# Optimization experiments

Hardware: AMD Instinct MI355X
Metric: run time of the kernel (lower is better)

Reference implementation:

```python
import jax, jax.numpy as jnp
import numpy as np

ROBOT_W = 1.0
PHASE_W = 1.0
COHER_W = 10.0
SPEED_W = 5.0
MAX_SPEED = 10.0
SMOOTH_VEL_W = 0.05
SMOOTH_ACC_W = 0.01

# illegal phase transitions {(0,2),(1,0),(2,0),(2,1)} as a 3x3 lookup table
_ILLEGAL = np.zeros((3, 3), dtype=bool)
for a, b in [(0, 2), (1, 0), (2, 0), (2, 1)]:
    _ILLEGAL[a, b] = True
ILLEGAL_TABLE = jnp.asarray(_ILLEGAL)


def setup_inputs() -> dict:
    key = jax.random.key(0)
    k1, k2, k3, k4 = jax.random.split(key, 4)
    B, T = 256, 8192
    # scale by 8 so per-frame speeds (norm of diffs of 3-vectors) exceed MAX_SPEED
    pred_robot = jax.random.normal(k1, (B, T, 12), dtype=jnp.float32) * 8.0
    gt_robot = jax.random.normal(k2, (B, T, 12), dtype=jnp.float32) * 8.0
    pred_phase = jax.random.normal(k3, (B, T, 3), dtype=jnp.float32)
    gt_phase = jax.random.randint(k4, (B, T), 0, 3, dtype=jnp.int32)
    return {"pred_robot": pred_robot, "pred_phase": pred_phase,
            "gt_robot": gt_robot, "gt_phase": gt_phase}


def _coherence_loss(phase_logits):
    # vectorized replacement for the O(B*T) Python double loop
    p = jnp.argmax(phase_logits, axis=-1)            # [B, T]
    pt, pt1 = p[:, :-1], p[:, 1:]                    # [B, T-1]
    illegal = ILLEGAL_TABLE[pt, pt1]                 # [B, T-1] bool
    # logit of the (illegal) predicted phase at t+1
    sel = jnp.take_along_axis(phase_logits[:, 1:], pt1[..., None], axis=-1)[..., 0]
    loss_sum = jnp.sum(jnp.where(illegal, sel * sel, 0.0))
    count = jnp.sum(illegal)
    return jnp.where(count > 0, loss_sum / jnp.maximum(count, 1).astype(sel.dtype), 0.0)


def _speed_loss(pred_robot):
    B, T, D = pred_robot.shape
    vel = pred_robot[:, 1:] - pred_robot[:, :-1]     # [B, T-1, 12]
    pts = vel.reshape(B, T - 1, 4, 3)
    speeds = jnp.linalg.norm(pts, axis=-1)           # [B, T-1, 4]
    pen = jax.nn.relu(speeds - MAX_SPEED)
    return SPEED_W * jnp.mean(pen * pen)


def reference(pred_robot, pred_phase, gt_robot, gt_phase):
    # MSE over robot trajectory
    robot_loss = jnp.mean((pred_robot - gt_robot) ** 2)
    # cross-entropy over 3 phase classes
    logp = jax.nn.log_softmax(pred_phase, axis=-1)   # [B, T, 3]
    nll = -jnp.take_along_axis(logp, gt_phase[..., None].astype(jnp.int32), axis=-1)[..., 0]
    phase_loss = jnp.mean(nll)
    coherence = _coherence_loss(pred_phase)
    speed_loss = _speed_loss(pred_robot)
    vel = pred_robot[:, 1:] - pred_robot[:, :-1]
    vel_loss = jnp.mean(vel * vel)
    acc = pred_robot[:, 2:] - 2.0 * pred_robot[:, 1:-1] + pred_robot[:, :-2]
    acc_loss = jnp.mean(acc * acc)
    total = (ROBOT_W * robot_loss + PHASE_W * phase_loss + COHER_W * coherence
             + speed_loss + SMOOTH_VEL_W * vel_loss + SMOOTH_ACC_W * acc_loss)
    return total
```

## Files before the change

### kernel.cpp

```cpp
#include <hip/hip_runtime.h>
#include <math.h>

#define B_DIM 256
#define T_DIM 8192
#define BLOCK 256
#define NSLOT 256
#define K_PRED 4
#define NPB (BLOCK * K_PRED)
#define NF4 (B_DIM * T_DIM * 3)
#define NPH4 (NF4 / 4)
#define GRID_BLOCKS (NF4 / NPB)


__device__ __forceinline__ unsigned div3u(unsigned x) {
    return __umulhi(x, 0xAAAAAAABu) >> 1;
}
__device__ __forceinline__ float pen_term(float s) {
    float d = fmaxf(sqrtf(s) - 10.0f, 0.0f);
    return d * d;
}
__device__ __forceinline__ void argmax3(float l0, float l1, float l2, int &p, float &m) {
    p = 0; m = l0;
    if (l1 > m) { m = l1; p = 1; }
    if (l2 > m) { m = l2; p = 2; }
}
__device__ __forceinline__ float nll3(float l0, float l1, float l2, int g) {
    float mx = fmaxf(l0, fmaxf(l1, l2));
    float s = __expf(l0 - mx) + __expf(l1 - mx) + __expf(l2 - mx);
    float sel = (g == 0) ? l0 : ((g == 1) ? l1 : l2);
    return mx + __logf(s) - sel;
}

__global__ __launch_bounds__(BLOCK, 3) void combined_loss_main(
    const float4* __restrict__ pred4,
    const float4* __restrict__ ph4,
    const float4* __restrict__ gt4,
    const int*    __restrict__ gt_phase,
    double* __restrict__ ws)
{
    __shared__ float  s_carry[NPB + 1];
    __shared__ float2 s_zw[BLOCK + 1];
    __shared__ float  s_pm_m[BLOCK + 1];
    __shared__ int    s_pm_p[BLOCK + 1];
    __shared__ float  s_red[4][6];

    const int tid = threadIdx.x;
    const int blk = blockIdx.x;
    const unsigned base = (unsigned)blk * NPB;
    const unsigned j = (unsigned)blk * BLOCK + tid;


    float2 zwp_s = make_float2(0.f, 0.f);
    float4 Ab = make_float4(0.f,0.f,0.f,0.f), Ab3 = Ab;
    unsigned cb = 0; bool carry_sent = false;
    if (tid == 0) {
        if (j != 0) zwp_s = ((const float2*)ph4)[2u * j - 1u];
        const unsigned ib = base + NPB;
        if (ib < (unsigned)NF4) {
            const unsigned rb = div3u(ib);
            cb = ib - 3u * rb;
            if ((rb & (T_DIM - 1)) < (T_DIM - 1)) {
                carry_sent = true;
                Ab  = pred4[ib];
                Ab3 = pred4[ib + 3u];
            }
        }
    }
    float4 Pn = make_float4(0.f,0.f,0.f,0.f);
    bool pn_valid = false;
    if (tid == BLOCK - 1) {
        if (j + 1u < (unsigned)NPH4) { pn_valid = true; Pn = ph4[j + 1u]; }
    }

    float4 A[K_PRED], G[K_PRED], A3[K_PRED], A6[K_PRED];
    unsigned cc[K_PRED];
    bool vv1[K_PRED], vv2[K_PRED];
    #pragma unroll
    for (int k = 0; k < K_PRED; ++k) {
        const unsigned i = base + (unsigned)(k * BLOCK) + tid;
        const unsigned r = div3u(i);
        cc[k] = i - 3u * r;
        const unsigned t = r & (T_DIM - 1);
        vv1[k] = t < (T_DIM - 1);
        vv2[k] = t < (T_DIM - 2);
        const unsigned ia = vv1[k] ? i + 3u : i;
        const unsigned ic = vv2[k] ? i + 6u : i;
        A[k]  = pred4[i];
        G[k]  = gt4[i];
        A3[k] = pred4[ia];
        A6[k] = pred4[ic];
    }

    const float4 P = ph4[j];
    const unsigned g   = div3u(j);
    const unsigned dph = j - 3u * g;
    const unsigned prow = 4u * g + dph;
    int gA, gB = 0;
    if (dph == 2) {
        const int2 gg = ((const int2*)gt_phase)[prow >> 1];
        gA = gg.x; gB = gg.y;
    } else {
        gA = gt_phase[prow];
    }


    float sse = 0.f, velsq = 0.f, accsq = 0.f;
    float loc[K_PRED], car[K_PRED];
    #pragma unroll
    for (int k = 0; k < K_PRED; ++k) {
        float d;
        d = A[k].x - G[k].x; sse = fmaf(d, d, sse);
        d = A[k].y - G[k].y; sse = fmaf(d, d, sse);
        d = A[k].z - G[k].z; sse = fmaf(d, d, sse);
        d = A[k].w - G[k].w; sse = fmaf(d, d, sse);

        float sqx = 0.f, sqy = 0.f, sqz = 0.f, sqw = 0.f;
        if (vv1[k]) {
            const float vx = A3[k].x - A[k].x, vy = A3[k].y - A[k].y;
            const float vz = A3[k].z - A[k].z, vw = A3[k].w - A[k].w;
            sqx = vx * vx; sqy = vy * vy; sqz = vz * vz; sqw = vw * vw;
            velsq += sqx + sqy + sqz + sqw;
        }
        if (vv2[k]) {
            float a;
            a = A6[k].x - 2.0f * A3[k].x + A[k].x; accsq = fmaf(a, a, accsq);
            a = A6[k].y - 2.0f * A3[k].y + A[k].y; accsq = fmaf(a, a, accsq);
            a = A6[k].z - 2.0f * A3[k].z + A[k].z; accsq = fmaf(a, a, accsq);
            a = A6[k].w - 2.0f * A3[k].w + A[k].w; accsq = fmaf(a, a, accsq);
        }
        float l3v, crv;
        const unsigned c = cc[k];
        if (c == 0)      { l3v = sqx + sqy + sqz; crv = sqw; }
        else if (c == 1) { l3v = sqz + sqw;       crv = sqx + sqy; }
        else             { l3v = sqy + sqz + sqw; crv = sqx; }
        loc[k] = l3v; car[k] = crv;
        s_carry[k * BLOCK + tid] = crv;
    }

    s_zw[tid + 1] = make_float2(P.z, P.w);
    if (tid == 0) {
        s_zw[0] = zwp_s;
        float crs = 0.f;
        if (carry_sent) {
            const float bx = Ab3.x - Ab.x, by = Ab3.y - Ab.y;
            const float bz = Ab3.z - Ab.z, bw = Ab3.w - Ab.w;
            const float sx = bx * bx, sy = by * by, sw = bw * bw;
            (void)bz;
            crs = (cb == 0) ? sw : ((cb == 1) ? (sx + sy) : sx);
        }
        s_carry[NPB] = crs;
    }
    __syncthreads();

    const float2 zwp = s_zw[tid];
    float l0, l1, l2;
    if (dph == 0)      { l0 = P.x;   l1 = P.y;   l2 = P.z; }
    else if (dph == 1) { l0 = zwp.y; l1 = P.x;   l2 = P.y; }
    else               { l0 = zwp.x; l1 = zwp.y; l2 = P.x; }

    float nll = nll3(l0, l1, l2, gA);
    int pP; float mP;
    argmax3(l0, l1, l2, pP, mP);
    s_pm_m[tid] = mP; s_pm_p[tid] = pP;

    int p3 = 0; float m3 = 0.f;
    if (dph == 2) {
        nll += nll3(P.y, P.z, P.w, gB);
        argmax3(P.y, P.z, P.w, p3, m3);
    }
    if (tid == BLOCK - 1) {
        float mS = 0.f; int pS = 0;
        if (pn_valid) {
            const unsigned jn = j + 1u;
            const unsigned gn = div3u(jn);
            const unsigned dn = jn - 3u * gn;
            float a0, a1, a2;
            if (dn == 0)      { a0 = Pn.x; a1 = Pn.y; a2 = Pn.z; }
            else if (dn == 1) { a0 = P.w;  a1 = Pn.x; a2 = Pn.y; }
            else              { a0 = P.z;  a1 = P.w;  a2 = Pn.x; }
            argmax3(a0, a1, a2, pS, mS);
        }
        s_pm_m[BLOCK] = mS; s_pm_p[BLOCK] = pS;
    }
    __syncthreads();

    float csum = 0.f, ccnt = 0.f;
    {
        const float mN = s_pm_m[tid + 1];
        const int   pN = s_pm_p[tid + 1];
        const unsigned t1 = prow & (T_DIM - 1);
        if (t1 < (T_DIM - 1)) {
            const int   pB2 = (dph == 2) ? p3 : pN;
            const float mB2 = (dph == 2) ? m3 : mN;
            const int mask = (pP == 0) ? 4 : ((pP == 1) ? 1 : 3);
            if ((mask >> pB2) & 1) { csum += mB2 * mB2; ccnt += 1.f; }
        }
        if (dph == 2) {
            const unsigned t2 = (prow + 1u) & (T_DIM - 1);
            if (t2 < (T_DIM - 1)) {
                const int mask = (p3 == 0) ? 4 : ((p3 == 1) ? 1 : 3);
                if ((mask >> pN) & 1) { csum += mN * mN; ccnt += 1.f; }
            }
        }
    }

    float pen2 = 0.f;
    #pragma unroll
    for (int k = 0; k < K_PRED; ++k) {
        unsigned ck = cc[k];
        const float up = s_carry[k * BLOCK + tid + 1];
        const float a = loc[k] + ((ck == 1u) ? up : 0.f);
        const float b = (ck == 0u) ? (car[k] + up) : 0.f;
        pen2 += pen_term(a) + pen_term(b);
    }

    float vals[6] = { fmaf(12.0f, nll, sse), csum, ccnt, pen2, velsq, accsq };
    #pragma unroll
    for (int off = 32; off > 0; off >>= 1) {
        #pragma unroll
        for (int q = 0; q < 6; ++q)
            vals[q] += __shfl_down(vals[q], off, 64);
    }
    const int wave = tid >> 6, lane = tid & 63;
    if (lane == 0) {
        #pragma unroll
        for (int q = 0; q < 6; ++q) s_red[wave][q] = vals[q];
    }
    __syncthreads();
    if (tid < 6) {
        const double acc = (double)s_red[0][tid] + (double)s_red[1][tid]
                         + (double)s_red[2][tid] + (double)s_red[3][tid];
        atomicAdd(&ws[(size_t)(blk & (NSLOT - 1)) * 8 + tid], acc);
    }
}

__global__ __launch_bounds__(256) void combined_loss_final(
    const double* __restrict__ ws, float* __restrict__ out)
{
    __shared__ double sred[4][6];
    const int tid = threadIdx.x;
    double v[6];
    #pragma unroll
    for (int q = 0; q < 6; ++q) v[q] = ws[(size_t)tid * 8 + q];
    #pragma unroll
    for (int off = 32; off > 0; off >>= 1) {
        #pragma unroll
        for (int q = 0; q < 6; ++q)
            v[q] += __shfl_down(v[q], off, 64);
    }
    const int wave = tid >> 6, lane = tid & 63;
    if (lane == 0) {
        #pragma unroll
        for (int q = 0; q < 6; ++q) sred[wave][q] = v[q];
    }
    __syncthreads();
    if (tid == 0) {
        double s[6];
        #pragma unroll
        for (int q = 0; q < 6; ++q)
            s[q] = sred[0][q] + sred[1][q] + sred[2][q] + sred[3][q];
        const double robot_phase = s[0] / (double)((size_t)B_DIM * T_DIM * 12);
        const double coher = (s[2] > 0.0) ? (s[1] / fmax(s[2], 1.0)) : 0.0;
        const double speed = 5.0  * (s[3] / (double)((size_t)B_DIM * (T_DIM - 1) * 4));
        const double vel   = 0.05 * (s[4] / (double)((size_t)B_DIM * (T_DIM - 1) * 12));
        const double acc   = 0.01 * (s[5] / (double)((size_t)B_DIM * (T_DIM - 2) * 12));
        out[0] = (float)(robot_phase + 10.0 * coher + speed + vel + acc);
    }
}

extern "C" void kernel_launch(void* const* d_in, const int* in_sizes, int n_in,
                              void* d_out, int out_size, void* d_ws, size_t ws_size,
                              hipStream_t stream)
{
    const float4* pred4      = (const float4*)d_in[0];
    const float4* ph4        = (const float4*)d_in[1];
    const float4* gt4        = (const float4*)d_in[2];
    const int*    gt_phase   = (const int*)d_in[3];
    double* ws  = (double*)d_ws;
    float*  out = (float*)d_out;

    hipMemsetAsync(d_ws, 0, (size_t)NSLOT * 8 * sizeof(double), stream);

    combined_loss_main<<<dim3(GRID_BLOCKS), BLOCK, 0, stream>>>(pred4, ph4, gt4, gt_phase, ws);
    combined_loss_final<<<1, 256, 0, stream>>>(ws, out);
}
```

Measured before the change: 239.4 us.

## Split fused loss kernel into separate robot and phase block roles

The single kernel now launches two kinds of blocks. One kind handles the robot trajectory terms (MSE, velocity, acceleration, speed penalty) with half as many rows per block, and the other handles the phase terms (NLL, coherence). Shared memory is aliased between the two roles and the occupancy hint goes from 3 to 8 blocks per CU. This aims to shorten per-block critical paths and raise occupancy for better latency hiding, at the cost of more blocks, more atomics and extra barriers.

```diff
diff --git a/kernel.cpp b/kernel.cpp
--- a/kernel.cpp
+++ b/kernel.cpp
@@ -5,11 +5,14 @@
 #define T_DIM 8192
 #define BLOCK 256
 #define NSLOT 256
-#define K_PRED 4
+#define ROWS_TOT (B_DIM * T_DIM)
+#define NF4  (ROWS_TOT * 3)
+#define NPH4 (NF4 / 4)
+#define K_PRED 2
 #define NPB (BLOCK * K_PRED)
-#define NF4 (B_DIM * T_DIM * 3)
-#define NPH4 (NF4 / 4)
-#define GRID_BLOCKS (NF4 / NPB)
+#define NB_PRED (NF4 / NPB)
+#define NB_PH   (NPH4 / BLOCK)
+#define GRID_BLOCKS (NB_PRED + NB_PH)
 
 
 __device__ __forceinline__ unsigned div3u(unsigned x) {
@@ -31,206 +34,227 @@
     return mx + __logf(s) - sel;
 }
 
-__global__ __launch_bounds__(BLOCK, 3) void combined_loss_main(
+__device__ __forceinline__ void reduce_and_emit(float vals[6], int tid, int blk,
+                                                float s_red[4][6], double* ws)
+{
+    #pragma unroll
+    for (int off = 32; off > 0; off >>= 1) {
+        #pragma unroll
+        for (int q = 0; q < 6; ++q)
+            vals[q] += __shfl_down(vals[q], off, 64);
+    }
+    const int wave = tid >> 6, lane = tid & 63;
+    if (lane == 0) {
+        #pragma unroll
+        for (int q = 0; q < 6; ++q) s_red[wave][q] = vals[q];
+    }
+    __syncthreads();
+    if (tid < 6) {
+        const double acc = (double)s_red[0][tid] + (double)s_red[1][tid]
+                         + (double)s_red[2][tid] + (double)s_red[3][tid];
+        atomicAdd(&ws[(size_t)(blk & (NSLOT - 1)) * 8 + tid], acc);
+    }
+}
+
+__global__ __launch_bounds__(BLOCK, 8) void combined_loss_main(
     const float4* __restrict__ pred4,
     const float4* __restrict__ ph4,
     const float4* __restrict__ gt4,
     const int*    __restrict__ gt_phase,
     double* __restrict__ ws)
 {
-    __shared__ float  s_carry[NPB + 1];
-    __shared__ float2 s_zw[BLOCK + 1];
-    __shared__ float  s_pm_m[BLOCK + 1];
-    __shared__ int    s_pm_p[BLOCK + 1];
-    __shared__ float  s_red[4][6];
+    __shared__ float s_xchg[NPB + 1];
+    __shared__ float s_red[4][6];
 
     const int tid = threadIdx.x;
     const int blk = blockIdx.x;
-    const unsigned base = (unsigned)blk * NPB;
-    const unsigned j = (unsigned)blk * BLOCK + tid;
-
-
-    float2 zwp_s = make_float2(0.f, 0.f);
-    float4 Ab = make_float4(0.f,0.f,0.f,0.f), Ab3 = Ab;
-    unsigned cb = 0; bool carry_sent = false;
-    if (tid == 0) {
-        if (j != 0) zwp_s = ((const float2*)ph4)[2u * j - 1u];
-        const unsigned ib = base + NPB;
-        if (ib < (unsigned)NF4) {
-            const unsigned rb = div3u(ib);
-            cb = ib - 3u * rb;
-            if ((rb & (T_DIM - 1)) < (T_DIM - 1)) {
-                carry_sent = true;
-                Ab  = pred4[ib];
-                Ab3 = pred4[ib + 3u];
-            }
-        }
-    }
-    float4 Pn = make_float4(0.f,0.f,0.f,0.f);
-    bool pn_valid = false;
-    if (tid == BLOCK - 1) {
-        if (j + 1u < (unsigned)NPH4) { pn_valid = true; Pn = ph4[j + 1u]; }
-    }
-
-    float4 A[K_PRED], G[K_PRED], A3[K_PRED], A6[K_PRED];
-    unsigned cc[K_PRED];
-    bool vv1[K_PRED], vv2[K_PRED];
-    #pragma unroll
-    for (int k = 0; k < K_PRED; ++k) {
-        const unsigned i = base + (unsigned)(k * BLOCK) + tid;
-        const unsigned r = div3u(i);
-        cc[k] = i - 3u * r;
-        const unsigned t = r & (T_DIM - 1);
-        vv1[k] = t < (T_DIM - 1);
-        vv2[k] = t < (T_DIM - 2);
-        const unsigned ia = vv1[k] ? i + 3u : i;
-        const unsigned ic = vv2[k] ? i + 6u : i;
-        A[k]  = pred4[i];
-        G[k]  = gt4[i];
-        A3[k] = pred4[ia];
-        A6[k] = pred4[ic];
-    }
-
-    const float4 P = ph4[j];
-    const unsigned g   = div3u(j);
-    const unsigned dph = j - 3u * g;
-    const unsigned prow = 4u * g + dph;
-    int gA, gB = 0;
-    if (dph == 2) {
-        const int2 gg = ((const int2*)gt_phase)[prow >> 1];
-        gA = gg.x; gB = gg.y;
+
+    if (blk < NB_PRED) {
+        const unsigned base = (unsigned)blk * NPB;
+
+        float4 Ab = make_float4(0.f,0.f,0.f,0.f), Ab3 = Ab;
+        unsigned cb = 0; bool carry_sent = false;
+        if (tid == 0) {
+            const unsigned ib = base + NPB;
+            if (ib < (unsigned)NF4) {
+                const unsigned rb = div3u(ib);
+                cb = ib - 3u * rb;
+                if ((rb & (T_DIM - 1)) < (T_DIM - 1)) {
+                    carry_sent = true;
+                    Ab  = pred4[ib];
+                    Ab3 = pred4[ib + 3u];
+                }
+            }
+        }
+
+        unsigned idx[K_PRED], i3[K_PRED], i6[K_PRED], cc[K_PRED];
+        bool vv1[K_PRED], vv2[K_PRED];
+        #pragma unroll
+        for (int k = 0; k < K_PRED; ++k) {
+            const unsigned i = base + (unsigned)(k * BLOCK) + tid;
+            const unsigned r = div3u(i);
+            cc[k] = i - 3u * r;
+            const unsigned t = r & (T_DIM - 1);
+            vv1[k] = t < (T_DIM - 1);
+            vv2[k] = t < (T_DIM - 2);
+            idx[k] = i;
+            i3[k] = vv1[k] ? i + 3u : i;
+            i6[k] = vv2[k] ? i + 6u : i;
+        }
+        float4 A[K_PRED], G[K_PRED], A3[K_PRED], A6[K_PRED];
+        #pragma unroll
+        for (int k = 0; k < K_PRED; ++k) {
+            A[k]  = pred4[idx[k]];
+            G[k]  = gt4[idx[k]];
+            A3[k] = pred4[i3[k]];
+            A6[k] = pred4[i6[k]];
+        }
+
+        float sse = 0.f, velsq = 0.f, accsq = 0.f;
+        float loc[K_PRED], car[K_PRED];
+        #pragma unroll
+        for (int k = 0; k < K_PRED; ++k) {
+            float d;
+            d = A[k].x - G[k].x; sse = fmaf(d, d, sse);
+            d = A[k].y - G[k].y; sse = fmaf(d, d, sse);
+            d = A[k].z - G[k].z; sse = fmaf(d, d, sse);
+            d = A[k].w - G[k].w; sse = fmaf(d, d, sse);
+
+            float sqx = 0.f, sqy = 0.f, sqz = 0.f, sqw = 0.f;
+            if (vv1[k]) {
+                const float vx = A3[k].x - A[k].x, vy = A3[k].y - A[k].y;
+                const float vz = A3[k].z - A[k].z, vw = A3[k].w - A[k].w;
+                sqx = vx * vx; sqy = vy * vy; sqz = vz * vz; sqw = vw * vw;
+                velsq += sqx + sqy + sqz + sqw;
+            }
+            if (vv2[k]) {
+                float a;
+                a = A6[k].x - 2.0f * A3[k].x + A[k].x; accsq = fmaf(a, a, accsq);
+                a = A6[k].y - 2.0f * A3[k].y + A[k].y; accsq = fmaf(a, a, accsq);
+                a = A6[k].z - 2.0f * A3[k].z + A[k].z; accsq = fmaf(a, a, accsq);
+                a = A6[k].w - 2.0f * A3[k].w + A[k].w; accsq = fmaf(a, a, accsq);
+            }
+            float l3v, crv;
+            const unsigned c = cc[k];
+            if (c == 0)      { l3v = sqx + sqy + sqz; crv = sqw; }
+            else if (c == 1) { l3v = sqz + sqw;       crv = sqx + sqy; }
+            else             { l3v = sqy + sqz + sqw; crv = sqx; }
+            loc[k] = l3v; car[k] = crv;
+            s_xchg[k * BLOCK + tid] = crv;
+        }
+        if (tid == 0) {
+            float crs = 0.f;
+            if (carry_sent) {
+                const float bx = Ab3.x - Ab.x, by = Ab3.y - Ab.y;
+                const float bz = Ab3.z - Ab.z, bw = Ab3.w - Ab.w;
+                const float sx = bx * bx, sy = by * by, sw = bw * bw;
+                (void)bz;
+                crs = (cb == 0) ? sw : ((cb == 1) ? (sx + sy) : sx);
+            }
+            s_xchg[NPB] = crs;
+        }
+        __syncthreads();
+
+        float pen2 = 0.f;
+        #pragma unroll
+        for (int k = 0; k < K_PRED; ++k) {
+            const unsigned ck = cc[k];
+            const float up = s_xchg[k * BLOCK + tid + 1];
+            const float a = loc[k] + ((ck == 1u) ? up : 0.f);
+            const float b = (ck == 0u) ? (car[k] + up) : 0.f;
+            pen2 += pen_term(a) + pen_term(b);
+        }
+        __syncthreads();
+
+        float vals[6] = { sse, 0.f, 0.f, pen2, velsq, accsq };
+        reduce_and_emit(vals, tid, blk, s_red, ws);
+
     } else {
-        gA = gt_phase[prow];
-    }
-
-
-    float sse = 0.f, velsq = 0.f, accsq = 0.f;
-    float loc[K_PRED], car[K_PRED];
-    #pragma unroll
-    for (int k = 0; k < K_PRED; ++k) {
-        float d;
-        d = A[k].x - G[k].x; sse = fmaf(d, d, sse);
-        d = A[k].y - G[k].y; sse = fmaf(d, d, sse);
-        d = A[k].z - G[k].z; sse = fmaf(d, d, sse);
-        d = A[k].w - G[k].w; sse = fmaf(d, d, sse);
-
-        float sqx = 0.f, sqy = 0.f, sqz = 0.f, sqw = 0.f;
-        if (vv1[k]) {
-            const float vx = A3[k].x - A[k].x, vy = A3[k].y - A[k].y;
-            const float vz = A3[k].z - A[k].z, vw = A3[k].w - A[k].w;
-            sqx = vx * vx; sqy = vy * vy; sqz = vz * vz; sqw = vw * vw;
-            velsq += sqx + sqy + sqz + sqw;
-        }
-        if (vv2[k]) {
-            float a;
-            a = A6[k].x - 2.0f * A3[k].x + A[k].x; accsq = fmaf(a, a, accsq);
-            a = A6[k].y - 2.0f * A3[k].y + A[k].y; accsq = fmaf(a, a, accsq);
-            a = A6[k].z - 2.0f * A3[k].z + A[k].z; accsq = fmaf(a, a, accsq);
-            a = A6[k].w - 2.0f * A3[k].w + A[k].w; accsq = fmaf(a, a, accsq);
-        }
-        float l3v, crv;
-        const unsigned c = cc[k];
-        if (c == 0)      { l3v = sqx + sqy + sqz; crv = sqw; }
-        else if (c == 1) { l3v = sqz + sqw;       crv = sqx + sqy; }
-        else             { l3v = sqy + sqz + sqw; crv = sqx; }
-        loc[k] = l3v; car[k] = crv;
-        s_carry[k * BLOCK + tid] = crv;
-    }
-
-    s_zw[tid + 1] = make_float2(P.z, P.w);
-    if (tid == 0) {
-        s_zw[0] = zwp_s;
-        float crs = 0.f;
-        if (carry_sent) {
-            const float bx = Ab3.x - Ab.x, by = Ab3.y - Ab.y;
-            const float bz = Ab3.z - Ab.z, bw = Ab3.w - Ab.w;
-            const float sx = bx * bx, sy = by * by, sw = bw * bw;
-            (void)bz;
-            crs = (cb == 0) ? sw : ((cb == 1) ? (sx + sy) : sx);
-        }
-        s_carry[NPB] = crs;
-    }
-    __syncthreads();
-
-    const float2 zwp = s_zw[tid];
-    float l0, l1, l2;
-    if (dph == 0)      { l0 = P.x;   l1 = P.y;   l2 = P.z; }
-    else if (dph == 1) { l0 = zwp.y; l1 = P.x;   l2 = P.y; }
-    else               { l0 = zwp.x; l1 = zwp.y; l2 = P.x; }
-
-    float nll = nll3(l0, l1, l2, gA);
-    int pP; float mP;
-    argmax3(l0, l1, l2, pP, mP);
-    s_pm_m[tid] = mP; s_pm_p[tid] = pP;
-
-    int p3 = 0; float m3 = 0.f;
-    if (dph == 2) {
-        nll += nll3(P.y, P.z, P.w, gB);
-        argmax3(P.y, P.z, P.w, p3, m3);
-    }
-    if (tid == BLOCK - 1) {
-        float mS = 0.f; int pS = 0;
-        if (pn_valid) {
-            const unsigned jn = j + 1u;
-            const unsigned gn = div3u(jn);
-            const unsigned dn = jn - 3u * gn;
-            float a0, a1, a2;
-            if (dn == 0)      { a0 = Pn.x; a1 = Pn.y; a2 = Pn.z; }
-            else if (dn == 1) { a0 = P.w;  a1 = Pn.x; a2 = Pn.y; }
-            else              { a0 = P.z;  a1 = P.w;  a2 = Pn.x; }
-            argmax3(a0, a1, a2, pS, mS);
-        }
-        s_pm_m[BLOCK] = mS; s_pm_p[BLOCK] = pS;
-    }
-    __syncthreads();
-
-    float csum = 0.f, ccnt = 0.f;
-    {
-        const float mN = s_pm_m[tid + 1];
-        const int   pN = s_pm_p[tid + 1];
-        const unsigned t1 = prow & (T_DIM - 1);
-        if (t1 < (T_DIM - 1)) {
-            const int   pB2 = (dph == 2) ? p3 : pN;
-            const float mB2 = (dph == 2) ? m3 : mN;
-            const int mask = (pP == 0) ? 4 : ((pP == 1) ? 1 : 3);
-            if ((mask >> pB2) & 1) { csum += mB2 * mB2; ccnt += 1.f; }
-        }
+        float2* s_zw  = (float2*)s_xchg;
+        float*  s_pm_m = s_xchg;
+        __shared__ int s_pm_p[BLOCK + 1];
+
+        const int pblk = blk - NB_PRED;
+        const unsigned j = (unsigned)pblk * BLOCK + tid;
+
+        float2 zwp_s = make_float2(0.f, 0.f);
+        if (tid == 0 && j != 0) zwp_s = ((const float2*)ph4)[2u * j - 1u];
+        float4 Pn = make_float4(0.f,0.f,0.f,0.f);
+        bool pn_valid = false;
+        if (tid == BLOCK - 1 && j + 1u < (unsigned)NPH4) { pn_valid = true; Pn = ph4[j + 1u]; }
+
+        const float4 P = ph4[j];
+        const unsigned g   = div3u(j);
+        const unsigned dph = j - 3u * g;
+        const unsigned prow = 4u * g + dph;
+        int gA, gB = 0;
         if (dph == 2) {
-            const unsigned t2 = (prow + 1u) & (T_DIM - 1);
-            if (t2 < (T_DIM - 1)) {
-                const int mask = (p3 == 0) ? 4 : ((p3 == 1) ? 1 : 3);
-                if ((mask >> pN) & 1) { csum += mN * mN; ccnt += 1.f; }
-            }
-        }
-    }
-
-    float pen2 = 0.f;
-    #pragma unroll
-    for (int k = 0; k < K_PRED; ++k) {
-        unsigned ck = cc[k];
-        const float up = s_carry[k * BLOCK + tid + 1];
-        const float a = loc[k] + ((ck == 1u) ? up : 0.f);
-        const float b = (ck == 0u) ? (car[k] + up) : 0.f;
-        pen2 += pen_term(a) + pen_term(b);
-    }
-
-    float vals[6] = { fmaf(12.0f, nll, sse), csum, ccnt, pen2, velsq, accsq };
-    #pragma unroll
-    for (int off = 32; off > 0; off >>= 1) {
-        #pragma unroll
-        for (int q = 0; q < 6; ++q)
-            vals[q] += __shfl_down(vals[q], off, 64);
-    }
-    const int wave = tid >> 6, lane = tid & 63;
-    if (lane == 0) {
-        #pragma unroll
-        for (int q = 0; q < 6; ++q) s_red[wave][q] = vals[q];
-    }
-    __syncthreads();
-    if (tid < 6) {
-        const double acc = (double)s_red[0][tid] + (double)s_red[1][tid]
-                         + (double)s_red[2][tid] + (double)s_red[3][tid];
-        atomicAdd(&ws[(size_t)(blk & (NSLOT - 1)) * 8 + tid], acc);
+            const int2 gg = ((const int2*)gt_phase)[prow >> 1];
+            gA = gg.x; gB = gg.y;
+        } else {
+            gA = gt_phase[prow];
+        }
+
+        s_zw[tid + 1] = make_float2(P.z, P.w);
+        if (tid == 0) s_zw[0] = zwp_s;
+        __syncthreads();
+
+        const float2 zwp = s_zw[tid];
+        float l0, l1, l2;
+        if (dph == 0)      { l0 = P.x;   l1 = P.y;   l2 = P.z; }
+        else if (dph == 1) { l0 = zwp.y; l1 = P.x;   l2 = P.y; }
+        else               { l0 = zwp.x; l1 = zwp.y; l2 = P.x; }
+
+        float nll = nll3(l0, l1, l2, gA);
+        int pP; float mP;
+        argmax3(l0, l1, l2, pP, mP);
+
+        int p3 = 0; float m3 = 0.f;
+        if (dph == 2) {
+            nll += nll3(P.y, P.z, P.w, gB);
+            argmax3(P.y, P.z, P.w, p3, m3);
+        }
+        __syncthreads();
+        s_pm_m[tid] = mP; s_pm_p[tid] = pP;
+        if (tid == BLOCK - 1) {
+            float mS = 0.f; int pS = 0;
+            if (pn_valid) {
+                const unsigned jn = j + 1u;
+                const unsigned gn = div3u(jn);
+                const unsigned dn = jn - 3u * gn;
+                float a0, a1, a2;
+                if (dn == 0)      { a0 = Pn.x; a1 = Pn.y; a2 = Pn.z; }
+                else if (dn == 1) { a0 = P.w;  a1 = Pn.x; a2 = Pn.y; }
+                else              { a0 = P.z;  a1 = P.w;  a2 = Pn.x; }
+                argmax3(a0, a1, a2, pS, mS);
+            }
+            s_pm_m[BLOCK] = mS; s_pm_p[BLOCK] = pS;
+        }
+        __syncthreads();
+
+        float csum = 0.f, ccnt = 0.f;
+        {
+            const float mN = s_pm_m[tid + 1];
+            const int   pN = s_pm_p[tid + 1];
+            const unsigned t1 = prow & (T_DIM - 1);
+            if (t1 < (T_DIM - 1)) {
+                const int   pB2 = (dph == 2) ? p3 : pN;
+                const float mB2 = (dph == 2) ? m3 : mN;
+                const int mask = (pP == 0) ? 4 : ((pP == 1) ? 1 : 3);
+                if ((mask >> pB2) & 1) { csum += mB2 * mB2; ccnt += 1.f; }
+            }
+            if (dph == 2) {
+                const unsigned t2 = (prow + 1u) & (T_DIM - 1);
+                if (t2 < (T_DIM - 1)) {
+                    const int mask = (p3 == 0) ? 4 : ((p3 == 1) ? 1 : 3);
+                    if ((mask >> pN) & 1) { csum += mN * mN; ccnt += 1.f; }
+                }
+            }
+        }
+        __syncthreads();
+
+        float vals[6] = { 12.0f * nll, csum, ccnt, 0.f, 0.f, 0.f };
+        reduce_and_emit(vals, tid, blk, s_red, ws);
     }
 }
 
```

Result: no change. 241.4 us (+0.8%).
